# Performance work log

Hardware: AMD Instinct MI355X
Metric: run time of the kernel (lower is better)

Reference implementation:

```python
import jax, jax.numpy as jnp
import numpy as np

EPS = 1e-8
DIGIT_TEMPERATURE = 1.0
SEED = 0
B, KMAX, V = 64, 16, 32000
DV, H = 10, 4096
# permute_prob table: prob_table[k] = permute_prob.get(k, 0.0)
_PROB = np.zeros(KMAX + 1, dtype=np.float32)
_PROB[2:] = 0.5
PROB_TABLE = jnp.asarray(_PROB)


def setup_inputs() -> dict:
    key = jax.random.key(0)
    ks = jax.random.split(key, 6)
    p_raw = jax.random.uniform(ks[0], (B, KMAX, V), dtype=jnp.float32)
    p_z = p_raw / p_raw.sum(axis=-1, keepdims=True)  # valid distributions per slot
    return {
        "p_z": p_z,
        "digit_logits_ref": jax.random.normal(ks[1], (B, DV), dtype=jnp.float32),
        "digit_logits_cf": jax.random.normal(ks[2], (B, DV), dtype=jnp.float32),
        "h_ans_ref": jax.random.normal(ks[3], (B, H), dtype=jnp.float32),
        "h_ans_cf": jax.random.normal(ks[4], (B, H), dtype=jnp.float32),
        "k_vals": jax.random.randint(ks[5], (B,), 0, KMAX + 1),
    }


def _js_divergence(p, q, eps=EPS):
    p = jnp.clip(p.astype(jnp.float32), eps)
    q = jnp.clip(q.astype(jnp.float32), eps)
    m = 0.5 * (p + q)
    log_m = jnp.log(m)
    kl_pm = (p * (jnp.log(p) - log_m)).sum(-1)
    kl_qm = (q * (jnp.log(q) - log_m)).sum(-1)
    return 0.5 * (kl_pm + kl_qm)


def _build_counterfactual_pz(p_z, k_vals):
    # Vectorized GS-mode counterfactual: per batch, with prob permute_prob[k]
    # (and k>1) permute the first k slots, otherwise temperature-warp them.
    bsz, kmax, vocab = p_z.shape
    key = jax.random.key(SEED)
    k_dec, k_perm, k_tau = jax.random.split(key, 3)
    u_dec = jax.random.uniform(k_dec, (bsz,))
    do_permute = (k_vals > 1) & (u_dec < PROB_TABLE[k_vals])  # [B]
    slots = jnp.arange(kmax)
    active = slots[None, :] < k_vals[:, None]  # [B, K]
    # ragged permutation of the first k slots: argsort random keys, inactive -> +inf
    u_perm = jax.random.uniform(k_perm, (bsz, kmax))
    perm = jnp.argsort(jnp.where(active, u_perm, jnp.inf), axis=1)  # stable: tail keeps order
    permuted = jnp.take_along_axis(p_z, perm[:, :, None], axis=1)
    # temperature warp: softmax(log(p)/tau), tau ~ U(0.7, 1.6) per slot
    tau = jax.random.uniform(k_tau, (bsz, kmax, 1), minval=0.7, maxval=1.6)
    warped = jax.nn.softmax(jnp.log(jnp.clip(p_z, EPS)) / tau, axis=-1)
    cf = jnp.where(do_permute[:, None, None], permuted, warped)
    return jnp.where(active[:, :, None], cf, p_z)


def reference(p_z, digit_logits_ref, digit_logits_cf, h_ans_ref, h_ans_cf, k_vals):
    p_cf_z = _build_counterfactual_pz(p_z, k_vals)
    # safe_softmax(logits, tau) == softmax(logits / tau)
    p_ref = jax.lax.stop_gradient(
        jax.nn.softmax(digit_logits_ref / DIGIT_TEMPERATURE, axis=-1))
    p_cf = jax.nn.softmax(digit_logits_cf / DIGIT_TEMPERATURE, axis=-1)
    js = _js_divergence(p_ref, p_cf).mean()
    loss_cf = jnp.log(jnp.float32(2.0)) - js
    ref_f = jax.lax.stop_gradient(h_ans_ref.astype(jnp.float32))
    cf_f = h_ans_cf.astype(jnp.float32)
    ref_norm = ref_f / jnp.clip(jnp.linalg.norm(ref_f, axis=-1, keepdims=True), 1e-12)
    cf_norm = cf_f / jnp.clip(jnp.linalg.norm(cf_f, axis=-1, keepdims=True), 1e-12)
    cos_sim = (ref_norm * cf_norm).sum(-1).mean()
    loss_dep = cos_sim - 1.0  # cf_mode == 'gs'
    dep_norm = jnp.linalg.norm(ref_f - cf_f, axis=-1).mean()
    return loss_cf, loss_dep, dep_norm, p_cf_z
```

## Files before the change

kernel.cpp:

```cpp
#include <hip/hip_runtime.h>
#include <stdint.h>

#define NB    64
#define KMAX  16
#define VV    32000
#define DVV   10
#define HH    4096
#define NROWS (NB*KMAX)
#define EPSF  1e-8f
#define NQ    8000

__device__ __forceinline__ uint32_t rotl32(uint32_t v, int r) { return (v << r) | (v >> (32 - r)); }

__device__ __forceinline__ void tf2x32(uint32_t k0, uint32_t k1, uint32_t c0, uint32_t c1,
                                       uint32_t& o0, uint32_t& o1) {
    uint32_t ks2 = k0 ^ k1 ^ 0x1BD11BDAu;
    uint32_t x0 = c0 + k0, x1 = c1 + k1;
    const int RA[4] = {13, 15, 26, 6};
    const int RB[4] = {17, 29, 16, 24};
#pragma unroll
    for (int i = 0; i < 4; ++i) { x0 += x1; x1 = rotl32(x1, RA[i]); x1 ^= x0; }
    x0 += k1; x1 += ks2 + 1u;
#pragma unroll
    for (int i = 0; i < 4; ++i) { x0 += x1; x1 = rotl32(x1, RB[i]); x1 ^= x0; }
    x0 += ks2; x1 += k0 + 2u;
#pragma unroll
    for (int i = 0; i < 4; ++i) { x0 += x1; x1 = rotl32(x1, RA[i]); x1 ^= x0; }
    x0 += k0; x1 += k1 + 3u;
#pragma unroll
    for (int i = 0; i < 4; ++i) { x0 += x1; x1 = rotl32(x1, RB[i]); x1 ^= x0; }
    x0 += k1; x1 += ks2 + 4u;
#pragma unroll
    for (int i = 0; i < 4; ++i) { x0 += x1; x1 = rotl32(x1, RA[i]); x1 ^= x0; }
    x0 += ks2; x1 += k0 + 5u;
    o0 = x0; o1 = x1;
}

__device__ __forceinline__ float bits_to_u01(uint32_t bits) {
    uint32_t fb = (bits >> 9) | 0x3F800000u;
    return __uint_as_float(fb) - 1.0f;
}

__global__ __launch_bounds__(1024) void setup_kernel(const int* __restrict__ k_vals,
                                                     int* __restrict__ src_arr,
                                                     float* __restrict__ itau_arr,
                                                     int* __restrict__ rowmap) {
    const int j = threadIdx.x;
    const int b = j >> 4, s = j & 15;

    __shared__ float su[NROWS];
    __shared__ int   sk[NB];
    __shared__ int   sdp[NB];
    __shared__ int   wcnt[16];
    __shared__ int   woff[17];

    uint32_t a0, b0, a1, b1, a2, b2;
    tf2x32(0u, 0u, 0u, 3u, a0, b0);
    tf2x32(0u, 0u, 1u, 4u, a1, b1);
    tf2x32(0u, 0u, 2u, 5u, a2, b2);
    const uint32_t kdec0 = a0, kdec1 = a1;
    const uint32_t kperm0 = a2, kperm1 = b0;
    const uint32_t ktau0 = b1, ktau1 = b2;

    uint32_t y0, y1, pb, tb;
    if (j < 512) { tf2x32(kperm0, kperm1, (uint32_t)j, (uint32_t)(j + 512), y0, y1); pb = y0; }
    else         { tf2x32(kperm0, kperm1, (uint32_t)(j - 512), (uint32_t)j, y0, y1); pb = y1; }
    su[j] = bits_to_u01(pb);
    if (j < 512) { tf2x32(ktau0, ktau1, (uint32_t)j, (uint32_t)(j + 512), y0, y1); tb = y0; }
    else         { tf2x32(ktau0, ktau1, (uint32_t)(j - 512), (uint32_t)j, y0, y1); tb = y1; }
    float tau = fmaxf(0.7f, bits_to_u01(tb) * 0.9f + 0.7f);
    float itau = 1.0f / tau;

    if (j < NB) {
        uint32_t bits;
        if (j < 32) { tf2x32(kdec0, kdec1, (uint32_t)j, (uint32_t)(j + 32), y0, y1); bits = y0; }
        else        { tf2x32(kdec0, kdec1, (uint32_t)(j - 32), (uint32_t)j, y0, y1); bits = y1; }
        float u_dec = bits_to_u01(bits);
        int k = k_vals[j];
        float prob = (k >= 2) ? 0.5f : 0.0f;
        sk[j] = k;
        sdp[j] = (k > 1) && (u_dec < prob);
    }
    __syncthreads();

    const int k = sk[b];
    const bool dp = sdp[b] != 0;
    const float INF = __int_as_float(0x7F800000);
    const float myk = (s < k) ? su[j] : INF;

    int r = 0;
#pragma unroll
    for (int t = 0; t < KMAX; ++t) {
        float kt = (t < k) ? su[(b << 4) + t] : INF;
        r += (kt < myk) || (kt == myk && t < s);
    }

    if (s >= k)      { src_arr[j] = s;            itau_arr[j] = 0.0f; }
    else if (dp)     { src_arr[(b << 4) + r] = s; itau_arr[(b << 4) + r] = 0.0f; }
    else             { src_arr[j] = -1;           itau_arr[j] = itau; }

    const bool iswarp = (s < k) && !dp;
    const uint64_t mask = __ballot(iswarp);
    const int lane = j & 63, w = j >> 6;
    const int lanePre = __popcll(mask & ((lane == 0) ? 0ull : (~0ull >> (64 - lane))));
    if (lane == 0) wcnt[w] = __popcll(mask);
    __syncthreads();
    if (j == 0) {
        woff[0] = 0;
        for (int i = 0; i < 16; ++i) woff[i + 1] = woff[i] + wcnt[i];
    }
    __syncthreads();
    const int nwarp = woff[16];
    const int wpre = woff[w] + lanePre;
    const int pos = iswarp ? wpre : nwarp + (j - wpre);
    rowmap[pos] = j;
}

__global__ __launch_bounds__(512) void cf_main_kernel(const float* __restrict__ p_z,
                                                      const int* __restrict__ src_arr,
                                                      const float* __restrict__ itau_arr,
                                                      const int* __restrict__ rowmap,
                                                      float* __restrict__ out) {
    const int row = rowmap[blockIdx.x];
    const int b = row >> 4;
    const int src = src_arr[row];
    const int tid = threadIdx.x;
    float* dst = out + (size_t)row * VV;

    if (src >= 0) {
        const float* sp = p_z + ((size_t)((b << 4) + src)) * VV;
#pragma unroll
        for (int i = 0; i < 16; ++i) {
            const int q = tid + (i << 9);
            if (q < NQ - 1) {
                float4 v = *(const float4*)(sp + (q << 2) + 1);
                *(float4*)(dst + (q << 2) + 1) = v;
            }
        }
        if (tid == 0) dst[0] = sp[0];
        if (tid == 1) {
            dst[VV - 3] = sp[VV - 3];
            dst[VV - 2] = sp[VV - 2];
            dst[VV - 1] = sp[VV - 1];
        }
        return;
    }

    const float it = itau_arr[row];
    const float* sp = p_z + (size_t)row * VV;
    float4 r[16];
    float e0 = 0.f, t0 = 0.f, t1 = 0.f, t2 = 0.f;
    float lsum = 0.f;
#pragma unroll
    for (int i = 0; i < 16; ++i) {
        const int q = tid + (i << 9);
        if (q < NQ - 1) {
            float4 v = *(const float4*)(sp + (q << 2) + 1);
            v.x = exp2f(__log2f(fmaxf(v.x, EPSF)) * it);
            v.y = exp2f(__log2f(fmaxf(v.y, EPSF)) * it);
            v.z = exp2f(__log2f(fmaxf(v.z, EPSF)) * it);
            v.w = exp2f(__log2f(fmaxf(v.w, EPSF)) * it);
            r[i] = v;
            lsum += v.x + v.y + v.z + v.w;
        } else {
            r[i] = make_float4(0.f, 0.f, 0.f, 0.f);
        }
    }
    if (tid == 0) { e0 = exp2f(__log2f(fmaxf(sp[0], EPSF)) * it); lsum += e0; }
    if (tid == 1) {
        t0 = exp2f(__log2f(fmaxf(sp[VV - 3], EPSF)) * it);
        t1 = exp2f(__log2f(fmaxf(sp[VV - 2], EPSF)) * it);
        t2 = exp2f(__log2f(fmaxf(sp[VV - 1], EPSF)) * it);
        lsum += t0 + t1 + t2;
    }
    __shared__ float red[8];
    float t = lsum;
#pragma unroll
    for (int o = 32; o; o >>= 1) t += __shfl_down(t, o, 64);
    if ((tid & 63) == 0) red[tid >> 6] = t;
    __syncthreads();
    if (tid < 64) {
        float u = (tid < 8) ? red[tid] : 0.0f;
#pragma unroll
        for (int o = 4; o; o >>= 1) u += __shfl_down(u, o, 64);
        if (tid == 0) red[0] = u;
    }
    __syncthreads();
    const float scale = 1.0f / red[0];

#pragma unroll
    for (int i = 0; i < 16; ++i) {
        const int q = tid + (i << 9);
        if (q < NQ - 1) {
            float4 st;
            st.x = r[i].x * scale; st.y = r[i].y * scale;
            st.z = r[i].z * scale; st.w = r[i].w * scale;
            *(float4*)(dst + (q << 2) + 1) = st;
        }
    }
    if (tid == 0) dst[0] = e0 * scale;
    if (tid == 1) {
        dst[VV - 3] = t0 * scale;
        dst[VV - 2] = t1 * scale;
        dst[VV - 1] = t2 * scale;
    }
}

__global__ __launch_bounds__(256) void rowred_kernel(const float* __restrict__ hr,
                                                     const float* __restrict__ hc,
                                                     float* __restrict__ cosb,
                                                     float* __restrict__ depb) {
    int b = blockIdx.x;
    const float4* r4 = (const float4*)(hr + (size_t)b * HH);
    const float4* c4 = (const float4*)(hc + (size_t)b * HH);
    float srr = 0.f, scc = 0.f, sxc = 0.f, sdd = 0.f;
    for (int i = threadIdx.x; i < HH / 4; i += 256) {
        float4 r = r4[i], c = c4[i];
        srr += r.x * r.x + r.y * r.y + r.z * r.z + r.w * r.w;
        scc += c.x * c.x + c.y * c.y + c.z * c.z + c.w * c.w;
        sxc += r.x * c.x + r.y * c.y + r.z * c.z + r.w * c.w;
        float dx = r.x - c.x, dy = r.y - c.y, dz = r.z - c.z, dw = r.w - c.w;
        sdd += dx * dx + dy * dy + dz * dz + dw * dw;
    }
#pragma unroll
    for (int o = 32; o; o >>= 1) {
        srr += __shfl_down(srr, o, 64);
        scc += __shfl_down(scc, o, 64);
        sxc += __shfl_down(sxc, o, 64);
        sdd += __shfl_down(sdd, o, 64);
    }
    __shared__ float red[4][4];
    int w = threadIdx.x >> 6;
    if ((threadIdx.x & 63) == 0) { red[w][0] = srr; red[w][1] = scc; red[w][2] = sxc; red[w][3] = sdd; }
    __syncthreads();
    if (threadIdx.x == 0) {
        float t0 = 0.f, t1 = 0.f, t2 = 0.f, t3 = 0.f;
        for (int i = 0; i < 4; ++i) { t0 += red[i][0]; t1 += red[i][1]; t2 += red[i][2]; t3 += red[i][3]; }
        float nr = fmaxf(sqrtf(t0), 1e-12f);
        float nc = fmaxf(sqrtf(t1), 1e-12f);
        cosb[b] = t2 / (nr * nc);
        depb[b] = sqrtf(t3);
    }
}

__global__ void finalize_kernel(const float* __restrict__ dlr, const float* __restrict__ dlc,
                                const float* __restrict__ cosb, const float* __restrict__ depb,
                                float* __restrict__ out) {
    int b = threadIdx.x;
    float lr[DVV], lc[DVV];
    float mr = -1e30f, mc = -1e30f;
#pragma unroll
    for (int v = 0; v < DVV; ++v) {
        lr[v] = dlr[b * DVV + v]; lc[v] = dlc[b * DVV + v];
        mr = fmaxf(mr, lr[v]); mc = fmaxf(mc, lc[v]);
    }
    float sr = 0.f, sc = 0.f;
#pragma unroll
    for (int v = 0; v < DVV; ++v) {
        lr[v] = expf(lr[v] - mr); sr += lr[v];
        lc[v] = expf(lc[v] - mc); sc += lc[v];
    }
    float js = 0.f;
#pragma unroll
    for (int v = 0; v < DVV; ++v) {
        float p = fmaxf(lr[v] / sr, EPSF);
        float q = fmaxf(lc[v] / sc, EPSF);
        float m = 0.5f * (p + q);
        float lm = logf(m);
        js += 0.5f * (p * (logf(p) - lm) + q * (logf(q) - lm));
    }
    float cs = cosb[b], dp = depb[b];
#pragma unroll
    for (int o = 32; o; o >>= 1) {
        js += __shfl_down(js, o, 64);
        cs += __shfl_down(cs, o, 64);
        dp += __shfl_down(dp, o, 64);
    }
    if (b == 0) {
        out[0] = logf(2.0f) - js * (1.0f / 64.0f);
        out[1] = cs * (1.0f / 64.0f) - 1.0f;
        out[2] = dp * (1.0f / 64.0f);
    }
}

extern "C" void kernel_launch(void* const* d_in, const int* in_sizes, int n_in,
                              void* d_out, int out_size, void* d_ws, size_t ws_size,
                              hipStream_t stream) {
    const float* p_z = (const float*)d_in[0];
    const float* dlr = (const float*)d_in[1];
    const float* dlc = (const float*)d_in[2];
    const float* hr  = (const float*)d_in[3];
    const float* hc  = (const float*)d_in[4];
    const int*   kv  = (const int*)d_in[5];
    float* out = (float*)d_out;

    int*   src_arr  = (int*)d_ws;
    float* itau_arr = (float*)d_ws + NROWS;
    int*   rowmap   = (int*)d_ws + 2 * NROWS;
    float* cosb     = (float*)d_ws + 3 * NROWS;
    float* depb     = cosb + NB;

    setup_kernel<<<1, 1024, 0, stream>>>(kv, src_arr, itau_arr, rowmap);
    cf_main_kernel<<<NROWS, 512, 0, stream>>>(p_z, src_arr, itau_arr, rowmap, out + 3);
    rowred_kernel<<<NB, 256, 0, stream>>>(hr, hc, cosb, depb);
    finalize_kernel<<<1, 64, 0, stream>>>(dlr, dlc, cosb, depb, out);
}
```

Before: 61.37 us.

## Fuse setup, row reductions and finalize into one kernel; widen main blocks, add nontemporal stores

Merges setup, per-batch hidden-state reductions and the final scalar computation into a single pre-kernel, using a last-block atomic ticket for the finalize step. This cuts four launches to two plus a memset. The main counterfactual kernel moves to 1024-thread blocks with 8 float4 per thread and writes output with nontemporal stores to avoid cache pollution. The added memset launch and the atomic/threadfence add a little overhead, and the larger blocks may lower occupancy.

Result: slower. 63.27 us (+3.1%).

```diff
diff --git a/kernel.cpp b/kernel.cpp
--- a/kernel.cpp
+++ b/kernel.cpp
@@ -10,6 +10,8 @@
 #define EPSF  1e-8f
 #define NQ    8000
 
+typedef float floatx4 __attribute__((ext_vector_type(4)));
+
 __device__ __forceinline__ uint32_t rotl32(uint32_t v, int r) { return (v << r) | (v >> (32 - r)); }
 
 __device__ __forceinline__ void tf2x32(uint32_t k0, uint32_t k1, uint32_t c0, uint32_t c1,
@@ -41,86 +43,176 @@
     return __uint_as_float(fb) - 1.0f;
 }
 
-__global__ __launch_bounds__(1024) void setup_kernel(const int* __restrict__ k_vals,
-                                                     int* __restrict__ src_arr,
-                                                     float* __restrict__ itau_arr,
-                                                     int* __restrict__ rowmap) {
-    const int j = threadIdx.x;
-    const int b = j >> 4, s = j & 15;
-
-    __shared__ float su[NROWS];
-    __shared__ int   sk[NB];
-    __shared__ int   sdp[NB];
-    __shared__ int   wcnt[16];
-    __shared__ int   woff[17];
-
-    uint32_t a0, b0, a1, b1, a2, b2;
-    tf2x32(0u, 0u, 0u, 3u, a0, b0);
-    tf2x32(0u, 0u, 1u, 4u, a1, b1);
-    tf2x32(0u, 0u, 2u, 5u, a2, b2);
-    const uint32_t kdec0 = a0, kdec1 = a1;
-    const uint32_t kperm0 = a2, kperm1 = b0;
-    const uint32_t ktau0 = b1, ktau1 = b2;
-
-    uint32_t y0, y1, pb, tb;
-    if (j < 512) { tf2x32(kperm0, kperm1, (uint32_t)j, (uint32_t)(j + 512), y0, y1); pb = y0; }
-    else         { tf2x32(kperm0, kperm1, (uint32_t)(j - 512), (uint32_t)j, y0, y1); pb = y1; }
-    su[j] = bits_to_u01(pb);
-    if (j < 512) { tf2x32(ktau0, ktau1, (uint32_t)j, (uint32_t)(j + 512), y0, y1); tb = y0; }
-    else         { tf2x32(ktau0, ktau1, (uint32_t)(j - 512), (uint32_t)j, y0, y1); tb = y1; }
-    float tau = fmaxf(0.7f, bits_to_u01(tb) * 0.9f + 0.7f);
-    float itau = 1.0f / tau;
-
-    if (j < NB) {
-        uint32_t bits;
-        if (j < 32) { tf2x32(kdec0, kdec1, (uint32_t)j, (uint32_t)(j + 32), y0, y1); bits = y0; }
-        else        { tf2x32(kdec0, kdec1, (uint32_t)(j - 32), (uint32_t)j, y0, y1); bits = y1; }
-        float u_dec = bits_to_u01(bits);
-        int k = k_vals[j];
-        float prob = (k >= 2) ? 0.5f : 0.0f;
-        sk[j] = k;
-        sdp[j] = (k > 1) && (u_dec < prob);
-    }
+__device__ __forceinline__ void nt_store4(float* p, float a, float b, float c, float d) {
+    floatx4 v = {a, b, c, d};
+    __builtin_nontemporal_store(v, (floatx4*)p);
+}
+
+__global__ __launch_bounds__(1024) void pre_kernel(const int* __restrict__ k_vals,
+                                                   const float* __restrict__ dlr,
+                                                   const float* __restrict__ dlc,
+                                                   const float* __restrict__ hr,
+                                                   const float* __restrict__ hc,
+                                                   int* __restrict__ src_arr,
+                                                   float* __restrict__ itau_arr,
+                                                   int* __restrict__ rowmap,
+                                                   float* __restrict__ cosb,
+                                                   float* __restrict__ depb,
+                                                   int* __restrict__ counter,
+                                                   float* __restrict__ out) {
+    if (blockIdx.x == 0) {
+        const int j = threadIdx.x;
+        const int b = j >> 4, s = j & 15;
+
+        __shared__ float su[NROWS];
+        __shared__ int   sk[NB];
+        __shared__ int   sdp[NB];
+        __shared__ int   wcnt[16];
+        __shared__ int   woff[17];
+
+        uint32_t a0, b0, a1, b1, a2, b2;
+        tf2x32(0u, 0u, 0u, 3u, a0, b0);
+        tf2x32(0u, 0u, 1u, 4u, a1, b1);
+        tf2x32(0u, 0u, 2u, 5u, a2, b2);
+        const uint32_t kdec0 = a0, kdec1 = a1;
+        const uint32_t kperm0 = a2, kperm1 = b0;
+        const uint32_t ktau0 = b1, ktau1 = b2;
+
+        uint32_t y0, y1, pb, tb;
+        if (j < 512) { tf2x32(kperm0, kperm1, (uint32_t)j, (uint32_t)(j + 512), y0, y1); pb = y0; }
+        else         { tf2x32(kperm0, kperm1, (uint32_t)(j - 512), (uint32_t)j, y0, y1); pb = y1; }
+        su[j] = bits_to_u01(pb);
+        if (j < 512) { tf2x32(ktau0, ktau1, (uint32_t)j, (uint32_t)(j + 512), y0, y1); tb = y0; }
+        else         { tf2x32(ktau0, ktau1, (uint32_t)(j - 512), (uint32_t)j, y0, y1); tb = y1; }
+        float tau = fmaxf(0.7f, bits_to_u01(tb) * 0.9f + 0.7f);
+        float itau = 1.0f / tau;
+
+        if (j < NB) {
+            uint32_t bits;
+            if (j < 32) { tf2x32(kdec0, kdec1, (uint32_t)j, (uint32_t)(j + 32), y0, y1); bits = y0; }
+            else        { tf2x32(kdec0, kdec1, (uint32_t)(j - 32), (uint32_t)j, y0, y1); bits = y1; }
+            float u_dec = bits_to_u01(bits);
+            int k = k_vals[j];
+            float prob = (k >= 2) ? 0.5f : 0.0f;
+            sk[j] = k;
+            sdp[j] = (k > 1) && (u_dec < prob);
+        }
+        __syncthreads();
+
+        const int k = sk[b];
+        const bool dp = sdp[b] != 0;
+        const float INF = __int_as_float(0x7F800000);
+        const float myk = (s < k) ? su[j] : INF;
+
+        int r = 0;
+#pragma unroll
+        for (int t = 0; t < KMAX; ++t) {
+            float kt = (t < k) ? su[(b << 4) + t] : INF;
+            r += (kt < myk) || (kt == myk && t < s);
+        }
+
+        if (s >= k)      { src_arr[j] = s;            itau_arr[j] = 0.0f; }
+        else if (dp)     { src_arr[(b << 4) + r] = s; itau_arr[(b << 4) + r] = 0.0f; }
+        else             { src_arr[j] = -1;           itau_arr[j] = itau; }
+
+        const bool iswarp = (s < k) && !dp;
+        const uint64_t mask = __ballot(iswarp);
+        const int lane = j & 63, w = j >> 6;
+        const int lanePre = __popcll(mask & ((lane == 0) ? 0ull : (~0ull >> (64 - lane))));
+        if (lane == 0) wcnt[w] = __popcll(mask);
+        __syncthreads();
+        if (j == 0) {
+            woff[0] = 0;
+            for (int i = 0; i < 16; ++i) woff[i + 1] = woff[i] + wcnt[i];
+        }
+        __syncthreads();
+        const int nwarp = woff[16];
+        const int wpre = woff[w] + lanePre;
+        const int pos = iswarp ? wpre : nwarp + (j - wpre);
+        rowmap[pos] = j;
+        return;
+    }
+
+    const int b = blockIdx.x - 1;
+    const int tid = threadIdx.x;
+    const float4* r4 = (const float4*)(hr + (size_t)b * HH);
+    const float4* c4 = (const float4*)(hc + (size_t)b * HH);
+    float4 rr = r4[tid], cc = c4[tid];
+    float srr = rr.x * rr.x + rr.y * rr.y + rr.z * rr.z + rr.w * rr.w;
+    float scc = cc.x * cc.x + cc.y * cc.y + cc.z * cc.z + cc.w * cc.w;
+    float sxc = rr.x * cc.x + rr.y * cc.y + rr.z * cc.z + rr.w * cc.w;
+    float dx = rr.x - cc.x, dy = rr.y - cc.y, dz = rr.z - cc.z, dw = rr.w - cc.w;
+    float sdd = dx * dx + dy * dy + dz * dz + dw * dw;
+#pragma unroll
+    for (int o = 32; o; o >>= 1) {
+        srr += __shfl_down(srr, o, 64);
+        scc += __shfl_down(scc, o, 64);
+        sxc += __shfl_down(sxc, o, 64);
+        sdd += __shfl_down(sdd, o, 64);
+    }
+    __shared__ float red[16][4];
+    __shared__ int s_ticket;
+    const int w = tid >> 6;
+    if ((tid & 63) == 0) { red[w][0] = srr; red[w][1] = scc; red[w][2] = sxc; red[w][3] = sdd; }
     __syncthreads();
-
-    const int k = sk[b];
-    const bool dp = sdp[b] != 0;
-    const float INF = __int_as_float(0x7F800000);
-    const float myk = (s < k) ? su[j] : INF;
-
-    int r = 0;
-#pragma unroll
-    for (int t = 0; t < KMAX; ++t) {
-        float kt = (t < k) ? su[(b << 4) + t] : INF;
-        r += (kt < myk) || (kt == myk && t < s);
-    }
-
-    if (s >= k)      { src_arr[j] = s;            itau_arr[j] = 0.0f; }
-    else if (dp)     { src_arr[(b << 4) + r] = s; itau_arr[(b << 4) + r] = 0.0f; }
-    else             { src_arr[j] = -1;           itau_arr[j] = itau; }
-
-    const bool iswarp = (s < k) && !dp;
-    const uint64_t mask = __ballot(iswarp);
-    const int lane = j & 63, w = j >> 6;
-    const int lanePre = __popcll(mask & ((lane == 0) ? 0ull : (~0ull >> (64 - lane))));
-    if (lane == 0) wcnt[w] = __popcll(mask);
+    if (tid == 0) {
+        float t0 = 0.f, t1 = 0.f, t2 = 0.f, t3 = 0.f;
+        for (int i = 0; i < 16; ++i) { t0 += red[i][0]; t1 += red[i][1]; t2 += red[i][2]; t3 += red[i][3]; }
+        float nr = fmaxf(sqrtf(t0), 1e-12f);
+        float nc = fmaxf(sqrtf(t1), 1e-12f);
+        cosb[b] = t2 / (nr * nc);
+        depb[b] = sqrtf(t3);
+        __threadfence();
+        s_ticket = atomicAdd(counter, 1);
+    }
     __syncthreads();
-    if (j == 0) {
-        woff[0] = 0;
-        for (int i = 0; i < 16; ++i) woff[i + 1] = woff[i] + wcnt[i];
-    }
-    __syncthreads();
-    const int nwarp = woff[16];
-    const int wpre = woff[w] + lanePre;
-    const int pos = iswarp ? wpre : nwarp + (j - wpre);
-    rowmap[pos] = j;
-}
-
-__global__ __launch_bounds__(512) void cf_main_kernel(const float* __restrict__ p_z,
-                                                      const int* __restrict__ src_arr,
-                                                      const float* __restrict__ itau_arr,
-                                                      const int* __restrict__ rowmap,
-                                                      float* __restrict__ out) {
+    if (s_ticket != NB - 1) return;
+    __threadfence();
+
+    if (tid < 64) {
+        const int bb = tid;
+        float lr[DVV], lc[DVV];
+        float mr = -1e30f, mc = -1e30f;
+#pragma unroll
+        for (int v = 0; v < DVV; ++v) {
+            lr[v] = dlr[bb * DVV + v]; lc[v] = dlc[bb * DVV + v];
+            mr = fmaxf(mr, lr[v]); mc = fmaxf(mc, lc[v]);
+        }
+        float sr = 0.f, sc = 0.f;
+#pragma unroll
+        for (int v = 0; v < DVV; ++v) {
+            lr[v] = expf(lr[v] - mr); sr += lr[v];
+            lc[v] = expf(lc[v] - mc); sc += lc[v];
+        }
+        float js = 0.f;
+#pragma unroll
+        for (int v = 0; v < DVV; ++v) {
+            float p = fmaxf(lr[v] / sr, EPSF);
+            float q = fmaxf(lc[v] / sc, EPSF);
+            float m = 0.5f * (p + q);
+            float lm = logf(m);
+            js += 0.5f * (p * (logf(p) - lm) + q * (logf(q) - lm));
+        }
+        float cs = cosb[bb], dpv = depb[bb];
+#pragma unroll
+        for (int o = 32; o; o >>= 1) {
+            js += __shfl_down(js, o, 64);
+            cs += __shfl_down(cs, o, 64);
+            dpv += __shfl_down(dpv, o, 64);
+        }
+        if (tid == 0) {
+            out[0] = logf(2.0f) - js * (1.0f / 64.0f);
+            out[1] = cs * (1.0f / 64.0f) - 1.0f;
+            out[2] = dpv * (1.0f / 64.0f);
+        }
+    }
+}
+
+__global__ __launch_bounds__(1024) void cf_main_kernel(const float* __restrict__ p_z,
+                                                       const int* __restrict__ src_arr,
+                                                       const float* __restrict__ itau_arr,
+                                                       const int* __restrict__ rowmap,
+                                                       float* __restrict__ out) {
     const int row = rowmap[blockIdx.x];
     const int b = row >> 4;
     const int src = src_arr[row];
@@ -130,11 +222,11 @@
     if (src >= 0) {
         const float* sp = p_z + ((size_t)((b << 4) + src)) * VV;
 #pragma unroll
-        for (int i = 0; i < 16; ++i) {
-            const int q = tid + (i << 9);
+        for (int i = 0; i < 8; ++i) {
+            const int q = tid + (i << 10);
             if (q < NQ - 1) {
                 float4 v = *(const float4*)(sp + (q << 2) + 1);
-                *(float4*)(dst + (q << 2) + 1) = v;
+                nt_store4(dst + (q << 2) + 1, v.x, v.y, v.z, v.w);
             }
         }
         if (tid == 0) dst[0] = sp[0];
@@ -148,12 +240,12 @@
 
     const float it = itau_arr[row];
     const float* sp = p_z + (size_t)row * VV;
-    float4 r[16];
+    float4 r[8];
     float e0 = 0.f, t0 = 0.f, t1 = 0.f, t2 = 0.f;
     float lsum = 0.f;
 #pragma unroll
-    for (int i = 0; i < 16; ++i) {
-        const int q = tid + (i << 9);
+    for (int i = 0; i < 8; ++i) {
+        const int q = tid + (i << 10);
         if (q < NQ - 1) {
             float4 v = *(const float4*)(sp + (q << 2) + 1);
             v.x = exp2f(__log2f(fmaxf(v.x, EPSF)) * it);
@@ -173,29 +265,27 @@
         t2 = exp2f(__log2f(fmaxf(sp[VV - 1], EPSF)) * it);
         lsum += t0 + t1 + t2;
     }
-    __shared__ float red[8];
+    __shared__ float red[16];
     float t = lsum;
 #pragma unroll
     for (int o = 32; o; o >>= 1) t += __shfl_down(t, o, 64);
     if ((tid & 63) == 0) red[tid >> 6] = t;
     __syncthreads();
     if (tid < 64) {
-        float u = (tid < 8) ? red[tid] : 0.0f;
-#pragma unroll
-        for (int o = 4; o; o >>= 1) u += __shfl_down(u, o, 64);
+        float u = (tid < 16) ? red[tid] : 0.0f;
+#pragma unroll
+        for (int o = 8; o; o >>= 1) u += __shfl_down(u, o, 64);
         if (tid == 0) red[0] = u;
     }
     __syncthreads();
     const float scale = 1.0f / red[0];
 
 #pragma unroll
-    for (int i = 0; i < 16; ++i) {
-        const int q = tid + (i << 9);
+    for (int i = 0; i < 8; ++i) {
+        const int q = tid + (i << 10);
         if (q < NQ - 1) {
-            float4 st;
-            st.x = r[i].x * scale; st.y = r[i].y * scale;
-            st.z = r[i].z * scale; st.w = r[i].w * scale;
-            *(float4*)(dst + (q << 2) + 1) = st;
+            nt_store4(dst + (q << 2) + 1,
+                      r[i].x * scale, r[i].y * scale, r[i].z * scale, r[i].w * scale);
         }
     }
     if (tid == 0) dst[0] = e0 * scale;
@@ -203,83 +293,6 @@
         dst[VV - 3] = t0 * scale;
         dst[VV - 2] = t1 * scale;
         dst[VV - 1] = t2 * scale;
-    }
-}
-
-__global__ __launch_bounds__(256) void rowred_kernel(const float* __restrict__ hr,
-                                                     const float* __restrict__ hc,
-                                                     float* __restrict__ cosb,
-                                                     float* __restrict__ depb) {
-    int b = blockIdx.x;
-    const float4* r4 = (const float4*)(hr + (size_t)b * HH);
-    const float4* c4 = (const float4*)(hc + (size_t)b * HH);
-    float srr = 0.f, scc = 0.f, sxc = 0.f, sdd = 0.f;
-    for (int i = threadIdx.x; i < HH / 4; i += 256) {
-        float4 r = r4[i], c = c4[i];
-        srr += r.x * r.x + r.y * r.y + r.z * r.z + r.w * r.w;
-        scc += c.x * c.x + c.y * c.y + c.z * c.z + c.w * c.w;
-        sxc += r.x * c.x + r.y * c.y + r.z * c.z + r.w * c.w;
-        float dx = r.x - c.x, dy = r.y - c.y, dz = r.z - c.z, dw = r.w - c.w;
-        sdd += dx * dx + dy * dy + dz * dz + dw * dw;
-    }
-#pragma unroll
-    for (int o = 32; o; o >>= 1) {
-        srr += __shfl_down(srr, o, 64);
-        scc += __shfl_down(scc, o, 64);
-        sxc += __shfl_down(sxc, o, 64);
-        sdd += __shfl_down(sdd, o, 64);
-    }
-    __shared__ float red[4][4];
-    int w = threadIdx.x >> 6;
-    if ((threadIdx.x & 63) == 0) { red[w][0] = srr; red[w][1] = scc; red[w][2] = sxc; red[w][3] = sdd; }
-    __syncthreads();
-    if (threadIdx.x == 0) {
-        float t0 = 0.f, t1 = 0.f, t2 = 0.f, t3 = 0.f;
-        for (int i = 0; i < 4; ++i) { t0 += red[i][0]; t1 += red[i][1]; t2 += red[i][2]; t3 += red[i][3]; }
-        float nr = fmaxf(sqrtf(t0), 1e-12f);
-        float nc = fmaxf(sqrtf(t1), 1e-12f);
-        cosb[b] = t2 / (nr * nc);
-        depb[b] = sqrtf(t3);
-    }
-}
-
-__global__ void finalize_kernel(const float* __restrict__ dlr, const float* __restrict__ dlc,
-                                const float* __restrict__ cosb, const float* __restrict__ depb,
-                                float* __restrict__ out) {
-    int b = threadIdx.x;
-    float lr[DVV], lc[DVV];
-    float mr = -1e30f, mc = -1e30f;
-#pragma unroll
-    for (int v = 0; v < DVV; ++v) {
-        lr[v] = dlr[b * DVV + v]; lc[v] = dlc[b * DVV + v];
-        mr = fmaxf(mr, lr[v]); mc = fmaxf(mc, lc[v]);
-    }
-    float sr = 0.f, sc = 0.f;
-#pragma unroll
-    for (int v = 0; v < DVV; ++v) {
-        lr[v] = expf(lr[v] - mr); sr += lr[v];
-        lc[v] = expf(lc[v] - mc); sc += lc[v];
-    }
-    float js = 0.f;
-#pragma unroll
-    for (int v = 0; v < DVV; ++v) {
-        float p = fmaxf(lr[v] / sr, EPSF);
-        float q = fmaxf(lc[v] / sc, EPSF);
-        float m = 0.5f * (p + q);
-        float lm = logf(m);
-        js += 0.5f * (p * (logf(p) - lm) + q * (logf(q) - lm));
-    }
-    float cs = cosb[b], dp = depb[b];
-#pragma unroll
-    for (int o = 32; o; o >>= 1) {
-        js += __shfl_down(js, o, 64);
-        cs += __shfl_down(cs, o, 64);
-        dp += __shfl_down(dp, o, 64);
-    }
-    if (b == 0) {
-        out[0] = logf(2.0f) - js * (1.0f / 64.0f);
-        out[1] = cs * (1.0f / 64.0f) - 1.0f;
-        out[2] = dp * (1.0f / 64.0f);
     }
 }
 
@@ -299,9 +312,11 @@
     int*   rowmap   = (int*)d_ws + 2 * NROWS;
     float* cosb     = (float*)d_ws + 3 * NROWS;
     float* depb     = cosb + NB;
-
-    setup_kernel<<<1, 1024, 0, stream>>>(kv, src_arr, itau_arr, rowmap);
-    cf_main_kernel<<<NROWS, 512, 0, stream>>>(p_z, src_arr, itau_arr, rowmap, out + 3);
-    rowred_kernel<<<NB, 256, 0, stream>>>(hr, hc, cosb, depb);
-    finalize_kernel<<<1, 64, 0, stream>>>(dlr, dlc, cosb, depb, out);
-}
+    int*   counter  = (int*)(depb + NB);
+
+    hipMemsetAsync(counter, 0, sizeof(int), stream);
+    pre_kernel<<<NB + 1, 1024, 0, stream>>>(kv, dlr, dlc, hr, hc,
+                                            src_arr, itau_arr, rowmap,
+                                            cosb, depb, counter, out);
+    cf_main_kernel<<<NROWS, 1024, 0, stream>>>(p_z, src_arr, itau_arr, rowmap, out + 3);
+}
```
